# Kernel optimization log

Measured on AMD Instinct MI355X. Metric: run time of the kernel, lower is better.

Reference implementation:

```python
import jax, jax.numpy as jnp
import numpy as np
import math

N_HEADS = 4
GELU = lambda x: jax.nn.gelu(x, approximate=False)  # torch nn.GELU default = exact erf

def _ln(x, s, b):
    m = jnp.mean(x, axis=-1, keepdims=True)
    v = jnp.mean((x - m) ** 2, axis=-1, keepdims=True)
    return (x - m) * jax.lax.rsqrt(v + 1e-5) * s + b

def _fwd(materials, in_seq, proj_vars, param_vars, enc_w1, enc_b1, enc_w2, enc_b2, sos,
         tl_wq, tl_wk, tl_wv, tl_bq, tl_bk, tl_bv, tl_wo, tl_bo,
         tl_ln1s, tl_ln1b, tl_ln2s, tl_ln2b, tl_fw1, tl_fb1, tl_fw2, tl_fb2,
         pw1, pb1, pw2, pb2, pw3, pb3, pw4, pb4, pw5, pb5,
         ipw1, ipb1, ipw2, ipb2, hw1, hb1, hw2, hb2, hw3, hb3):
    B = in_seq.shape[0]
    # encoder input MLP: [B,S,1] -> [B,S,D]
    x = GELU(in_seq @ enc_w1 + enc_b1) @ enc_w2 + enc_b2
    x = jnp.concatenate([jnp.broadcast_to(sos, (B, 1, sos.shape[-1])), x], axis=1)
    S1, D = x.shape[1], x.shape[2]
    dh = D // N_HEADS
    # sinusoidal positional encoding
    pos = jnp.arange(S1, dtype=jnp.float32)[:, None]
    div = jnp.exp(jnp.arange(0, D, 2, dtype=jnp.float32) * (-math.log(10000.0) / D))
    ang = pos * div
    pe = jnp.stack([jnp.sin(ang), jnp.cos(ang)], axis=-1).reshape(S1, D)
    x = x + pe
    scale = 1.0 / math.sqrt(dh)
    # post-LN TransformerEncoder layers (torch default norm_first=False), eval mode (no dropout)
    for l in range(tl_wq.shape[0]):
        q = (x @ tl_wq[l] + tl_bq[l]).reshape(B, S1, N_HEADS, dh).transpose(0, 2, 1, 3)
        k = (x @ tl_wk[l] + tl_bk[l]).reshape(B, S1, N_HEADS, dh).transpose(0, 2, 1, 3)
        v = (x @ tl_wv[l] + tl_bv[l]).reshape(B, S1, N_HEADS, dh).transpose(0, 2, 1, 3)
        att = jax.nn.softmax(jnp.einsum('bhqd,bhkd->bhqk', q, k) * scale, axis=-1)
        o = jnp.einsum('bhqk,bhkd->bhqd', att, v).transpose(0, 2, 1, 3).reshape(B, S1, D)
        x = _ln(x + o @ tl_wo[l] + tl_bo[l], tl_ln1s[l], tl_ln1b[l])
        f = GELU(x @ tl_fw1[l] + tl_fb1[l]) @ tl_fw2[l] + tl_fb2[l]
        x = _ln(x + f, tl_ln2s[l], tl_ln2b[l])
    sos_out = x[:, 0]
    h = jnp.concatenate([proj_vars, sos_out], axis=1)
    for w, b in ((pw1, pb1), (pw2, pb2), (pw3, pb3), (pw4, pb4)):
        h = GELU(h @ w + b)
    proj_out = h @ pw5 + pb5
    pp = GELU(param_vars @ ipw1 + ipb1) @ ipw2 + ipb2
    mi = jnp.concatenate([pp, proj_out], axis=1)  # [B, output_features+param_vars]
    # MaterialHead mask-gather-MLP-scatter == run every tiny head densely, pick by material id
    h1 = GELU(jnp.einsum('bi,mio->mbo', mi, hw1) + hb1[:, None, :])
    h2 = GELU(jnp.einsum('mbi,mio->mbo', h1, hw2) + hb2[:, None, :])
    h3 = jnp.einsum('mbi,mio->mbo', h2, hw3) + hb3[:, None, :]  # [M,B,1]
    return h3[materials, jnp.arange(B)]  # [B,1]

def setup_inputs() -> dict:
    key = jax.random.key(0)
    ks = iter(jax.random.split(key, 64))
    def rn(shape, scale=0.05):
        return jax.random.normal(next(ks), shape, dtype=jnp.float32) * scale
    B, S, IN, EL, D, L, DFF = 64, 1024, 1, 48, 64, 3, 256
    PV, PP, OF, M = 3, 3, 24, 3
    IF = OF + PP
    return dict(
        in_seq=rn((B, S, IN), 1.0),
        proj_vars=rn((B, PV), 1.0),
        param_vars=rn((B, PP), 1.0),
        materials=jax.random.randint(next(ks), (B,), 0, M),
        enc_w1=rn((IN, EL)), enc_b1=rn((EL,)), enc_w2=rn((EL, D)), enc_b2=rn((D,)),
        sos=rn((1, 1, D)),
        tl_wq=rn((L, D, D)), tl_wk=rn((L, D, D)), tl_wv=rn((L, D, D)),
        tl_bq=rn((L, D)), tl_bk=rn((L, D)), tl_bv=rn((L, D)),
        tl_wo=rn((L, D, D)), tl_bo=rn((L, D)),
        tl_ln1s=jnp.ones((L, D)), tl_ln1b=jnp.zeros((L, D)),
        tl_ln2s=jnp.ones((L, D)), tl_ln2b=jnp.zeros((L, D)),
        tl_fw1=rn((L, D, DFF)), tl_fb1=rn((L, DFF)), tl_fw2=rn((L, DFF, D)), tl_fb2=rn((L, D)),
        pw1=rn((PV + D, 34)), pb1=rn((34,)), pw2=rn((34, 11)), pb2=rn((11,)),
        pw3=rn((11, 36)), pb3=rn((36,)), pw4=rn((36, 22)), pb4=rn((22,)),
        pw5=rn((22, OF)), pb5=rn((OF,)),
        ipw1=rn((PP, 3)), ipb1=rn((3,)), ipw2=rn((3, PP)), ipb2=rn((PP,)),
        hw1=rn((M, IF, 15)), hb1=rn((M, 15)), hw2=rn((M, 15, 18)), hb2=rn((M, 18)),
        hw3=rn((M, 18, 1)), hb3=rn((M, 1)),
    )

def reference(in_seq, proj_vars, param_vars, materials, enc_w1, enc_b1, enc_w2, enc_b2, sos,
              tl_wq, tl_wk, tl_wv, tl_bq, tl_bk, tl_bv, tl_wo, tl_bo,
              tl_ln1s, tl_ln1b, tl_ln2s, tl_ln2b, tl_fw1, tl_fb1, tl_fw2, tl_fb2,
              pw1, pb1, pw2, pb2, pw3, pb3, pw4, pb4, pw5, pb5,
              ipw1, ipb1, ipw2, ipb2, hw1, hb1, hw2, hb2, hw3, hb3):
    return _fwd(materials, in_seq, proj_vars, param_vars, enc_w1, enc_b1, enc_w2, enc_b2, sos,
                tl_wq, tl_wk, tl_wv, tl_bq, tl_bk, tl_bv, tl_wo, tl_bo,
                tl_ln1s, tl_ln1b, tl_ln2s, tl_ln2b, tl_fw1, tl_fb1, tl_fw2, tl_fb2,
                pw1, pb1, pw2, pb2, pw3, pb3, pw4, pb4, pw5, pb5,
                ipw1, ipb1, ipw2, ipb2, hw1, hb1, hw2, hb2, hw3, hb3)
```

## Files before the change

kernel.cpp:

```cpp
#include <hip/hip_runtime.h>
#include <hip/hip_bf16.h>
#include <math.h>

#define BB   64
#define SS   1024
#define S1C  1025
#define DD   64
#define NHD  4
#define NBH  (BB * NHD)
#define DHD  16
#define DFFC 256
#define NLAY 3
#define NTOK (BB * S1C)
#define SPAD 1056
#define TGRP2 9
#define FTQ   32
#define FT2   32
#define HPAD 264
#define OPAD 68
#define YPAD 72
#define QSCL 0.36067376022224085f

typedef const float* fp;
typedef __attribute__((ext_vector_type(8))) short bf16x8;
typedef __attribute__((ext_vector_type(4))) float f32x4;
typedef __attribute__((ext_vector_type(2))) unsigned int u32x2;
typedef __attribute__((ext_vector_type(4))) unsigned int u32x4;

#if __has_builtin(__builtin_amdgcn_exp2f)
#define RAW_EXP2(x) __builtin_amdgcn_exp2f(x)
#else
#define RAW_EXP2(x) __expf(0.6931471805599453f * (x))
#endif
#if __has_builtin(__builtin_amdgcn_rcpf)
#define RAW_RCP(x) __builtin_amdgcn_rcpf(x)
#else
#define RAW_RCP(x) (1.0f / (x))
#endif

__device__ __forceinline__ float gelu_exact(float x) {
    return 0.5f * x * (1.0f + erff(x * 0.7071067811865475f));
}
__device__ __forceinline__ float erf_fast(float x) {
    float ax = fabsf(x);
    float t = RAW_RCP(1.0f + 0.3275911f * ax);
    float p = t * (0.254829592f + t * (-0.284496736f + t * (1.421413741f +
              t * (-1.453152027f + t * 1.061405429f))));
    float e = RAW_EXP2(ax * ax * -1.4426950408889634f);
    float r = 1.0f - p * e;
    return copysignf(r, x);
}
__device__ __forceinline__ float gelu_fast(float x) {
    return 0.5f * x * (1.0f + erf_fast(x * 0.7071067811865475f));
}
__device__ __forceinline__ short f2b(float f) {
    unsigned u = __float_as_uint(f);
    return (short)((u + 0x7fffu + ((u >> 16) & 1u)) >> 16);
}
__device__ __forceinline__ short f2b_pos(float f) {
    return (short)((__float_as_uint(f) + 0x8000u) >> 16);
}

__device__ __forceinline__ u32x2 pack4exp(f32x4 c, bool valid) {
    unsigned a0 = __float_as_uint(valid ? RAW_EXP2(c[0]) : 0.f) + 0x8000u;
    unsigned a1 = __float_as_uint(valid ? RAW_EXP2(c[1]) : 0.f) + 0x8000u;
    unsigned a2 = __float_as_uint(valid ? RAW_EXP2(c[2]) : 0.f) + 0x8000u;
    unsigned a3 = __float_as_uint(valid ? RAW_EXP2(c[3]) : 0.f) + 0x8000u;
    return (u32x2){__builtin_amdgcn_perm(a1, a0, 0x07060302u),
                   __builtin_amdgcn_perm(a3, a2, 0x07060302u)};
}

__global__ __launch_bounds__(256) void k_wconv(
    fp wq, fp wk, fp wv, fp wo, fp w1, fp w2,
    short* __restrict__ wqkvT, short* __restrict__ woT,
    short* __restrict__ w1T, short* __restrict__ w2T)
{
    int l = blockIdx.y;
    int i = blockIdx.x * 256 + threadIdx.x;
    if (i < 12288) {
        int p = i >> 12, rem = i & 4095;
        int d = rem >> 6, j = rem & 63;
        fp src = (p == 0 ? wq : p == 1 ? wk : wv) + (size_t)l * 4096;
        float v = src[j * 64 + d];
        if (p == 0) v *= QSCL;
        wqkvT[(size_t)l * 12288 + i] = f2b(v);
    } else if (i < 16384) {
        int rem = i - 12288;
        woT[(size_t)l * 4096 + rem] = f2b(wo[(size_t)l * 4096 + (rem & 63) * 64 + (rem >> 6)]);
    } else if (i < 32768) {
        int rem = i - 16384;
        w1T[(size_t)l * 16384 + rem] = f2b(w1[(size_t)l * 16384 + (rem & 63) * 256 + (rem >> 6)]);
    } else {
        int rem = i - 32768;
        w2T[(size_t)l * 16384 + rem] = f2b(w2[(size_t)l * 16384 + (rem & 255) * 64 + (rem >> 8)]);
    }
}

__global__ __launch_bounds__(64) void k_zero(
    short* __restrict__ qb, short* __restrict__ kb, short* __restrict__ vbt)
{
    int bh = blockIdx.x, t = threadIdx.x;
    for (int i = t; i < 31 * 16; i += 64) {
        int r = i >> 4, c = i & 15;
        size_t idx = ((size_t)bh * SPAD + 1025 + r) * 16 + c;
        qb[idx] = 0; kb[idx] = 0;
    }
    for (int i = t; i < 16 * 31; i += 64) {
        int e = i / 31, c = i % 31;
        vbt[((size_t)bh * 16 + e) * SPAD + 1025 + c] = 0;
    }
}

__global__ __launch_bounds__(256) void k_encode(
    fp in_seq, fp enc_w1, fp enc_b1, fp enc_w2, fp enc_b2, fp sos,
    float* __restrict__ x, short* __restrict__ xb)
{
    int t = threadIdx.x;
    int w = t >> 6, d = t & 63;
    int tok = blockIdx.x * 4 + w;
    int b = tok / S1C, s = tok % S1C;
    __shared__ float e[4][48];
    float val;
    if (s == 0) {
        val = sos[d];
    } else {
        float tin = in_seq[b * SS + (s - 1)];
        if (d < 48) e[w][d] = gelu_fast(tin * enc_w1[d] + enc_b1[d]);
        float acc = enc_b2[d];
        for (int j = 0; j < 48; ++j) acc += e[w][j] * enc_w2[j * DD + d];
        val = acc;
    }
    int i2 = (d >> 1) * 2;
    float factor = RAW_EXP2((float)i2 * (-9.210340371976184f / 64.0f) * 1.4426950408889634f);
    float ang = (float)s * factor;
    val += (d & 1) ? __cosf(ang) : __sinf(ang);
    x[(size_t)tok * DD + d] = val;
    xb[(size_t)tok * DD + d] = f2b(val);
}

__global__ __launch_bounds__(256) void k_qkv(
    const short* __restrict__ xb, const short* __restrict__ wqkvT,
    fp bq, fp bk, fp bv,
    short* __restrict__ qb, short* __restrict__ kb, short* __restrict__ vbt)
{
    int blk = blockIdx.x, t = threadIdx.x;
    int tok0 = blk * FTQ;
    int w = t >> 6, l = t & 63;
    int quad = l >> 4, lo = l & 15;

    const short* xp0 = xb + ((size_t)(tok0 + lo)) * DD;
    const short* xp1 = xb + ((size_t)(tok0 + 16 + lo)) * DD;
    bf16x8 a0 = *(const bf16x8*)(xp0 + quad * 8);
    bf16x8 a1 = *(const bf16x8*)(xp0 + 32 + quad * 8);
    bf16x8 a2 = *(const bf16x8*)(xp1 + quad * 8);
    bf16x8 a3 = *(const bf16x8*)(xp1 + 32 + quad * 8);

    int n = w * 16 + lo;
    #pragma unroll
    for (int p = 0; p < 3; ++p) {
        const short* wT = wqkvT + (size_t)p * 4096 + (size_t)n * 64;
        bf16x8 b0 = *(const bf16x8*)(wT + quad * 8);
        bf16x8 b1 = *(const bf16x8*)(wT + 32 + quad * 8);
        f32x4 c0 = __builtin_amdgcn_mfma_f32_16x16x32_bf16(a0, b0, (f32x4){0,0,0,0}, 0, 0, 0);
        c0 = __builtin_amdgcn_mfma_f32_16x16x32_bf16(a1, b1, c0, 0, 0, 0);
        f32x4 c1 = __builtin_amdgcn_mfma_f32_16x16x32_bf16(a2, b0, (f32x4){0,0,0,0}, 0, 0, 0);
        c1 = __builtin_amdgcn_mfma_f32_16x16x32_bf16(a3, b1, c1, 0, 0, 0);
        float bias = (p == 0) ? bq[n] * QSCL : (p == 1) ? bk[n] : bv[n];
        #pragma unroll
        for (int r = 0; r < 4; ++r) {
            int tok = tok0 + quad * 4 + r;
            int bb0 = tok / S1C, ss0 = tok % S1C;
            int bh = bb0 * NHD + w;
            short val = f2b(c0[r] + bias);
            int tok2 = tok + 16;
            int bb1 = tok2 / S1C, ss1 = tok2 % S1C;
            int bh2 = bb1 * NHD + w;
            short val2 = f2b(c1[r] + bias);
            if (p == 0) {
                qb[((size_t)bh * SPAD + ss0) * 16 + lo] = val;
                qb[((size_t)bh2 * SPAD + ss1) * 16 + lo] = val2;
            } else if (p == 1) {
                kb[((size_t)bh * SPAD + ss0) * 16 + lo] = val;
                kb[((size_t)bh2 * SPAD + ss1) * 16 + lo] = val2;
            } else {
                vbt[((size_t)bh * 16 + lo) * SPAD + ss0] = val;
                vbt[((size_t)bh2 * 16 + lo) * SPAD + ss1] = val2;
            }
        }
    }
}

__global__ __launch_bounds__(256) void k_attn(
    const short* __restrict__ qb, const short* __restrict__ kb,
    const short* __restrict__ vbt, short* __restrict__ ob)
{
    int bid = blockIdx.x;
    int bh  = bid % NBH;
    int grp = bid / NBH;
    int b = bh >> 2, h = bh & 3;
    int t = threadIdx.x;
    int w = t >> 6, l = t & 63;
    int quad = l >> 4, lo = l & 15;
    int t0 = grp * 4 + w;
    int t1 = t0 + 36;
    if (t1 > 65) t1 = 65;
    int qg0 = t0 * 16, qg1 = t1 * 16;

    __shared__ u32x2 ptmem[4][2][272];
    char* ptc = (char*)&ptmem[w][0][0];
    unsigned ptbase = (unsigned)(uintptr_t)ptc;

    const short* qbase = qb + (size_t)bh * SPAD * 16;
    const short* kbase = kb + (size_t)bh * SPAD * 16;
    const short* vbase = vbt + (size_t)bh * 16 * SPAD;

    bf16x8 aQ0 = {0,0,0,0,0,0,0,0}, aQ1 = {0,0,0,0,0,0,0,0};
    if (quad < 2) {
        aQ0 = *(const bf16x8*)(qbase + ((size_t)(qg0 + lo)) * 16 + quad * 8);
        aQ1 = *(const bf16x8*)(qbase + ((size_t)(qg1 + lo)) * 16 + quad * 8);
    }

    const short ONE = 0x3F80;
    bf16x8 aOne = {ONE, ONE, ONE, ONE, ONE, ONE, ONE, ONE};

    f32x4 oc0 = {0.f,0.f,0.f,0.f}, oc1 = {0.f,0.f,0.f,0.f};
    f32x4 dn0 = {0.f,0.f,0.f,0.f}, dn1 = {0.f,0.f,0.f,0.f};

    unsigned wo0, wo1;
    { int k0 = lo;       wo0 = (unsigned)((k0 >> 2) * 136 + (k0 & 3) * 32 + quad * 8);
      int k1 = 16 + lo;  wo1 = (unsigned)((k1 >> 2) * 136 + (k1 & 3) * 32 + quad * 8); }
    unsigned ro = (unsigned)(quad * 272 + lo * 8);
    unsigned rd0 = ptbase + ro;
    unsigned rd1 = ptbase + 2176 + ro;
    char* wb0 = ptc;
    char* wb1 = ptc + 2176;

    bf16x8 kxA, kyA, kxB, kyB, vA, vB;

    {
        const short* k0p = kbase + (size_t)lo * 16 + (quad & 1) * 8;
        kxA = *(const bf16x8*)k0p;
        kyA = *(const bf16x8*)(k0p + 256);
        vA  = *(const bf16x8*)(vbase + (size_t)lo * SPAD + quad * 8);
        const short* k1p = kbase + (size_t)(32 + lo) * 16 + (quad & 1) * 8;
        kxB = *(const bf16x8*)k1p;
        kyB = *(const bf16x8*)(k1p + 256);

        f32x4 c0 = __builtin_amdgcn_mfma_f32_16x16x32_bf16(aQ0, kxA, (f32x4){0.f,0.f,0.f,0.f}, 0, 0, 0);
        f32x4 c1 = __builtin_amdgcn_mfma_f32_16x16x32_bf16(aQ1, kxA, (f32x4){0.f,0.f,0.f,0.f}, 0, 0, 0);
        *(u32x2*)(wb0 + wo0)        = pack4exp(c0, true);
        *(u32x2*)(wb0 + 1088 + wo0) = pack4exp(c1, true);
        c0 = __builtin_amdgcn_mfma_f32_16x16x32_bf16(aQ0, kyA, (f32x4){0.f,0.f,0.f,0.f}, 0, 0, 0);
        c1 = __builtin_amdgcn_mfma_f32_16x16x32_bf16(aQ1, kyA, (f32x4){0.f,0.f,0.f,0.f}, 0, 0, 0);
        *(u32x2*)(wb0 + wo1)        = pack4exp(c0, true);
        *(u32x2*)(wb0 + 1088 + wo1) = pack4exp(c1, true);
    }

#define STEP(CH, TAIL, KXC, KYC, KXN, KYN, VP, VC, RD, WB) do {               \
    int ch_ = (CH);                                                            \
    if (!(TAIL)) {                                                             \
        const short* kn_ = kbase + (size_t)((ch_ + 1) * 32 + lo) * 16 + (quad & 1) * 8; \
        KXN = *(const bf16x8*)kn_;                                             \
        KYN = *(const bf16x8*)(kn_ + 256);                                     \
    }                                                                          \
    VC = *(const bf16x8*)(vbase + (size_t)lo * SPAD + ch_ * 32 + quad * 8);    \
    asm volatile("s_waitcnt lgkmcnt(0)" ::: "memory");                         \
    u32x2 p00_, p01_, p10_, p11_;                                              \
    asm volatile("ds_read_b64_tr_b16 %0, %1"             : "=v"(p00_) : "v"(RD)); \
    asm volatile("ds_read_b64_tr_b16 %0, %1 offset:136"  : "=v"(p01_) : "v"(RD)); \
    asm volatile("ds_read_b64_tr_b16 %0, %1 offset:1088" : "=v"(p10_) : "v"(RD)); \
    asm volatile("ds_read_b64_tr_b16 %0, %1 offset:1224" : "=v"(p11_) : "v"(RD)); \
    u32x2 wA0_, wA1_, wB0_, wB1_;                                              \
    {                                                                          \
        f32x4 c0_ = __builtin_amdgcn_mfma_f32_16x16x32_bf16(aQ0, KXC, (f32x4){0.f,0.f,0.f,0.f}, 0, 0, 0); \
        f32x4 c1_ = __builtin_amdgcn_mfma_f32_16x16x32_bf16(aQ1, KXC, (f32x4){0.f,0.f,0.f,0.f}, 0, 0, 0); \
        bool v0_ = !(TAIL) || (lo == 0);                                       \
        wA0_ = pack4exp(c0_, v0_);                                             \
        wB0_ = pack4exp(c1_, v0_);                                             \
        c0_ = __builtin_amdgcn_mfma_f32_16x16x32_bf16(aQ0, KYC, (f32x4){0.f,0.f,0.f,0.f}, 0, 0, 0); \
        c1_ = __builtin_amdgcn_mfma_f32_16x16x32_bf16(aQ1, KYC, (f32x4){0.f,0.f,0.f,0.f}, 0, 0, 0); \
        bool v1_ = !(TAIL);                                                    \
        wA1_ = pack4exp(c0_, v1_);                                             \
        wB1_ = pack4exp(c1_, v1_);                                             \
    }                                                                          \
    asm volatile("s_waitcnt lgkmcnt(0)" ::: "memory");                         \
    __builtin_amdgcn_sched_barrier(0);                                         \
    u32x4 q0_; q0_[0] = p00_[0]; q0_[1] = p00_[1]; q0_[2] = p01_[0]; q0_[3] = p01_[1]; \
    u32x4 q1_; q1_[0] = p10_[0]; q1_[1] = p10_[1]; q1_[2] = p11_[0]; q1_[3] = p11_[1]; \
    bf16x8 pB0_ = __builtin_bit_cast(bf16x8, q0_);                             \
    bf16x8 pB1_ = __builtin_bit_cast(bf16x8, q1_);                             \
    oc0 = __builtin_amdgcn_mfma_f32_16x16x32_bf16(VP, pB0_, oc0, 0, 0, 0);     \
    dn0 = __builtin_amdgcn_mfma_f32_16x16x32_bf16(aOne, pB0_, dn0, 0, 0, 0);   \
    oc1 = __builtin_amdgcn_mfma_f32_16x16x32_bf16(VP, pB1_, oc1, 0, 0, 0);     \
    dn1 = __builtin_amdgcn_mfma_f32_16x16x32_bf16(aOne, pB1_, dn1, 0, 0, 0);   \
    *(u32x2*)((WB) + wo0)        = wA0_;                                       \
    *(u32x2*)((WB) + 1088 + wo0) = wB0_;                                       \
    *(u32x2*)((WB) + wo1)        = wA1_;                                       \
    *(u32x2*)((WB) + 1088 + wo1) = wB1_;                                       \
} while (0)

    for (int chp = 1; chp < 31; chp += 2) {
        STEP(chp,     0, kxA, kyA, kxB, kyB, vA, vB, rd0, wb1);
        STEP(chp + 1, 0, kxB, kyB, kxA, kyA, vB, vA, rd1, wb0);
    }
    STEP(31, 0, kxA, kyA, kxB, kyB, vA, vB, rd0, wb1);
    STEP(32, 1, kxB, kyB, kxA, kyA, vB, vA, rd1, wb0);
#undef STEP

    {
        asm volatile("s_waitcnt lgkmcnt(0)" ::: "memory");
        u32x2 p00, p01, p10, p11;
        asm volatile("ds_read_b64_tr_b16 %0, %1"             : "=v"(p00) : "v"(rd0));
        asm volatile("ds_read_b64_tr_b16 %0, %1 offset:136"  : "=v"(p01) : "v"(rd0));
        asm volatile("ds_read_b64_tr_b16 %0, %1 offset:1088" : "=v"(p10) : "v"(rd0));
        asm volatile("ds_read_b64_tr_b16 %0, %1 offset:1224" : "=v"(p11) : "v"(rd0));
        asm volatile("s_waitcnt lgkmcnt(0)" ::: "memory");
        __builtin_amdgcn_sched_barrier(0);
        u32x4 q0; q0[0] = p00[0]; q0[1] = p00[1]; q0[2] = p01[0]; q0[3] = p01[1];
        u32x4 q1; q1[0] = p10[0]; q1[1] = p10[1]; q1[2] = p11[0]; q1[3] = p11[1];
        bf16x8 pB0 = __builtin_bit_cast(bf16x8, q0);
        bf16x8 pB1 = __builtin_bit_cast(bf16x8, q1);
        oc0 = __builtin_amdgcn_mfma_f32_16x16x32_bf16(vA, pB0, oc0, 0, 0, 0);
        dn0 = __builtin_amdgcn_mfma_f32_16x16x32_bf16(aOne, pB0, dn0, 0, 0, 0);
        oc1 = __builtin_amdgcn_mfma_f32_16x16x32_bf16(vA, pB1, oc1, 0, 0, 0);
        dn1 = __builtin_amdgcn_mfma_f32_16x16x32_bf16(aOne, pB1, dn1, 0, 0, 0);
    }

    {
        int qrow = qg0 + lo;
        if (qrow < S1C) {
            float inv = 1.0f / dn0[0];
            unsigned p0 = (unsigned short)f2b(oc0[0] * inv) | ((unsigned)(unsigned short)f2b(oc0[1] * inv) << 16);
            unsigned p1 = (unsigned short)f2b(oc0[2] * inv) | ((unsigned)(unsigned short)f2b(oc0[3] * inv) << 16);
            *(uint2*)(ob + ((size_t)b * S1C + qrow) * DD + h * DHD + quad * 4) = make_uint2(p0, p1);
        }
    }
    {
        int qrow = qg1 + lo;
        if (qrow < S1C) {
            float inv = 1.0f / dn1[0];
            unsigned p0 = (unsigned short)f2b(oc1[0] * inv) | ((unsigned)(unsigned short)f2b(oc1[1] * inv) << 16);
            unsigned p1 = (unsigned short)f2b(oc1[2] * inv) | ((unsigned)(unsigned short)f2b(oc1[3] * inv) << 16);
            *(uint2*)(ob + ((size_t)b * S1C + qrow) * DD + h * DHD + quad * 4) = make_uint2(p0, p1);
        }
    }
}

__global__ __launch_bounds__(256) void k_block(
    const short* __restrict__ ob, float* __restrict__ x,
    const short* __restrict__ woT, fp bo, fp ln1s, fp ln1b,
    const short* __restrict__ w1T, fp b1, const short* __restrict__ w2T, fp b2,
    fp ln2s, fp ln2b,
    const short* __restrict__ wqkvTn, fp bqn, fp bkn, fp bvn,
    short* __restrict__ qb, short* __restrict__ kb, short* __restrict__ vbt,
    int has_next)
{
    int blk = blockIdx.x, t = threadIdx.x;
    int tok0 = blk * FT2;
    int w = t >> 6, l = t & 63;
    int quad = l >> 4, lo = l & 15;

    __shared__ float otf[FT2][OPAD];
    __shared__ short ys[FT2][YPAD];
    __shared__ short hid[FT2][HPAD];

    {
        const short* obp0 = ob + ((size_t)(tok0 + lo)) * DD;
        const short* obp1 = ob + ((size_t)(tok0 + 16 + lo)) * DD;
        bf16x8 a0 = *(const bf16x8*)(obp0 + quad * 8);
        bf16x8 a1 = *(const bf16x8*)(obp0 + 32 + quad * 8);
        bf16x8 a2 = *(const bf16x8*)(obp1 + quad * 8);
        bf16x8 a3 = *(const bf16x8*)(obp1 + 32 + quad * 8);
        int n = w * 16 + lo;
        const short* wT = woT + (size_t)n * 64;
        bf16x8 b0 = *(const bf16x8*)(wT + quad * 8);
        bf16x8 bb = *(const bf16x8*)(wT + 32 + quad * 8);
        f32x4 c0 = __builtin_amdgcn_mfma_f32_16x16x32_bf16(a0, b0, (f32x4){0,0,0,0}, 0, 0, 0);
        c0 = __builtin_amdgcn_mfma_f32_16x16x32_bf16(a1, bb, c0, 0, 0, 0);
        f32x4 c1 = __builtin_amdgcn_mfma_f32_16x16x32_bf16(a2, b0, (f32x4){0,0,0,0}, 0, 0, 0);
        c1 = __builtin_amdgcn_mfma_f32_16x16x32_bf16(a3, bb, c1, 0, 0, 0);
        float bov = bo[n];
        #pragma unroll
        for (int r = 0; r < 4; ++r) {
            otf[quad * 4 + r][n] = c0[r] + bov;
            otf[16 + quad * 4 + r][n] = c1[r] + bov;
        }
    }
    __syncthreads();

    int d = l;
    float yv[8];
    {
        float s1 = ln1s[d], bl1 = ln1b[d];
        #pragma unroll
        for (int i = 0; i < 8; ++i) {
            int tt = w * 8 + i;
            float val = otf[tt][d] + x[(size_t)(tok0 + tt) * DD + d];
            float sum = val, vs = val * val;
            #pragma unroll
            for (int off = 32; off > 0; off >>= 1) {
                sum += __shfl_xor(sum, off, 64);
                vs  += __shfl_xor(vs, off, 64);
            }
            float mean = sum * (1.0f / 64.0f);
            float var = vs * (1.0f / 64.0f) - mean * mean;
            float y = (val - mean) * rsqrtf(var + 1e-5f) * s1 + bl1;
            yv[i] = y;
            ys[tt][d] = f2b(y);
        }
    }
    __syncthreads();

    {
        bf16x8 a0 = *(const bf16x8*)&ys[lo][quad * 8];
        bf16x8 a1 = *(const bf16x8*)&ys[lo][32 + quad * 8];
        bf16x8 a2 = *(const bf16x8*)&ys[16 + lo][quad * 8];
        bf16x8 a3 = *(const bf16x8*)&ys[16 + lo][32 + quad * 8];
        #pragma unroll
        for (int i = 0; i < 4; ++i) {
            int n = w * 64 + i * 16 + lo;
            const short* wT = w1T + (size_t)n * 64;
            bf16x8 b0 = *(const bf16x8*)(wT + quad * 8);
            bf16x8 bb = *(const bf16x8*)(wT + 32 + quad * 8);
            f32x4 c0 = __builtin_amdgcn_mfma_f32_16x16x32_bf16(a0, b0, (f32x4){0,0,0,0}, 0, 0, 0);
            c0 = __builtin_amdgcn_mfma_f32_16x16x32_bf16(a1, bb, c0, 0, 0, 0);
            f32x4 c1 = __builtin_amdgcn_mfma_f32_16x16x32_bf16(a2, b0, (f32x4){0,0,0,0}, 0, 0, 0);
            c1 = __builtin_amdgcn_mfma_f32_16x16x32_bf16(a3, bb, c1, 0, 0, 0);
            float b1v = b1[n];
            #pragma unroll
            for (int r = 0; r < 4; ++r) {
                hid[quad * 4 + r][n] = f2b(gelu_fast(c0[r] + b1v));
                hid[16 + quad * 4 + r][n] = f2b(gelu_fast(c1[r] + b1v));
            }
        }
    }
    __syncthreads();

    {
        f32x4 c20 = {0.f,0.f,0.f,0.f}, c21 = {0.f,0.f,0.f,0.f};
        const short* wT2 = w2T + (size_t)(w * 16 + lo) * 256;
        #pragma unroll
        for (int kc = 0; kc < 8; ++kc) {
            bf16x8 b2f = *(const bf16x8*)(wT2 + kc * 32 + quad * 8);
            bf16x8 a20 = *(const bf16x8*)&hid[lo][kc * 32 + quad * 8];
            bf16x8 a21 = *(const bf16x8*)&hid[16 + lo][kc * 32 + quad * 8];
            c20 = __builtin_amdgcn_mfma_f32_16x16x32_bf16(a20, b2f, c20, 0, 0, 0);
            c21 = __builtin_amdgcn_mfma_f32_16x16x32_bf16(a21, b2f, c21, 0, 0, 0);
        }
        float b2v = b2[w * 16 + lo];
        #pragma unroll
        for (int r = 0; r < 4; ++r) {
            otf[quad * 4 + r][w * 16 + lo] = c20[r] + b2v;
            otf[16 + quad * 4 + r][w * 16 + lo] = c21[r] + b2v;
        }
    }
    __syncthreads();

    {
        float s2 = ln2s[d], bl2 = ln2b[d];
        #pragma unroll
        for (int i = 0; i < 8; ++i) {
            int tt = w * 8 + i;
            float val = otf[tt][d] + yv[i];
            float sum = val, vs = val * val;
            #pragma unroll
            for (int off = 32; off > 0; off >>= 1) {
                sum += __shfl_xor(sum, off, 64);
                vs  += __shfl_xor(vs, off, 64);
            }
            float mean = sum * (1.0f / 64.0f);
            float var = vs * (1.0f / 64.0f) - mean * mean;
            float y = (val - mean) * rsqrtf(var + 1e-5f) * s2 + bl2;
            x[(size_t)(tok0 + tt) * DD + d] = y;
            ys[tt][d] = f2b(y);
        }
    }
    __syncthreads();

    if (has_next) {
        bf16x8 a0 = *(const bf16x8*)&ys[lo][quad * 8];
        bf16x8 a1 = *(const bf16x8*)&ys[lo][32 + quad * 8];
        bf16x8 a2 = *(const bf16x8*)&ys[16 + lo][quad * 8];
        bf16x8 a3 = *(const bf16x8*)&ys[16 + lo][32 + quad * 8];
        int n = w * 16 + lo;
        #pragma unroll
        for (int p = 0; p < 3; ++p) {
            const short* wT = wqkvTn + (size_t)p * 4096 + (size_t)n * 64;
            bf16x8 b0 = *(const bf16x8*)(wT + quad * 8);
            bf16x8 bb = *(const bf16x8*)(wT + 32 + quad * 8);
            f32x4 c0 = __builtin_amdgcn_mfma_f32_16x16x32_bf16(a0, b0, (f32x4){0,0,0,0}, 0, 0, 0);
            c0 = __builtin_amdgcn_mfma_f32_16x16x32_bf16(a1, bb, c0, 0, 0, 0);
            f32x4 c1 = __builtin_amdgcn_mfma_f32_16x16x32_bf16(a2, b0, (f32x4){0,0,0,0}, 0, 0, 0);
            c1 = __builtin_amdgcn_mfma_f32_16x16x32_bf16(a3, bb, c1, 0, 0, 0);
            float bias = (p == 0) ? bqn[n] * QSCL : (p == 1) ? bkn[n] : bvn[n];
            #pragma unroll
            for (int r = 0; r < 4; ++r) {
                int tok = tok0 + quad * 4 + r;
                int bb0 = tok / S1C, ss0 = tok % S1C;
                int bh = bb0 * NHD + w;
                short val = f2b(c0[r] + bias);
                int tok2 = tok + 16;
                int bb1 = tok2 / S1C, ss1 = tok2 % S1C;
                int bh2 = bb1 * NHD + w;
                short val2 = f2b(c1[r] + bias);
                if (p == 0) {
                    qb[((size_t)bh * SPAD + ss0) * 16 + lo] = val;
                    qb[((size_t)bh2 * SPAD + ss1) * 16 + lo] = val2;
                } else if (p == 1) {
                    kb[((size_t)bh * SPAD + ss0) * 16 + lo] = val;
                    kb[((size_t)bh2 * SPAD + ss1) * 16 + lo] = val2;
                } else {
                    vbt[((size_t)bh * 16 + lo) * SPAD + ss0] = val;
                    vbt[((size_t)bh2 * 16 + lo) * SPAD + ss1] = val2;
                }
            }
        }
    }
}

__global__ __launch_bounds__(64) void k_head(
    const float* __restrict__ x, fp proj_vars, fp param_vars,
    const int* __restrict__ materials,
    fp pw1, fp pb1, fp pw2, fp pb2, fp pw3, fp pb3,
    fp pw4, fp pb4, fp pw5, fp pb5,
    fp ipw1, fp ipb1, fp ipw2, fp ipb2,
    fp hw1, fp hb1, fp hw2, fp hb2, fp hw3, fp hb3,
    float* __restrict__ out)
{
    int b = blockIdx.x;
    int tid = threadIdx.x;
    __shared__ float A[80], Bf[80], pp[8], mi[32];

    if (tid < 3) A[tid] = proj_vars[b * 3 + tid];
    A[3 + tid] = x[((size_t)b * S1C + 0) * DD + tid];
    __syncthreads();

    if (tid < 34) {
        float a = pb1[tid];
        for (int i = 0; i < 67; ++i) a += A[i] * pw1[i * 34 + tid];
        Bf[tid] = gelu_exact(a);
    }
    __syncthreads();
    if (tid < 11) {
        float a = pb2[tid];
        for (int i = 0; i < 34; ++i) a += Bf[i] * pw2[i * 11 + tid];
        A[tid] = gelu_exact(a);
    }
    __syncthreads();
    if (tid < 36) {
        float a = pb3[tid];
        for (int i = 0; i < 11; ++i) a += A[i] * pw3[i * 36 + tid];
        Bf[tid] = gelu_exact(a);
    }
    __syncthreads();
    if (tid < 22) {
        float a = pb4[tid];
        for (int i = 0; i < 36; ++i) a += Bf[i] * pw4[i * 22 + tid];
        A[tid] = gelu_exact(a);
    }
    __syncthreads();
    if (tid < 24) {
        float a = pb5[tid];
        for (int i = 0; i < 22; ++i) a += A[i] * pw5[i * 24 + tid];
        mi[3 + tid] = a;
    }
    if (tid < 3) {
        float a = ipb1[tid];
        for (int i = 0; i < 3; ++i) a += param_vars[b * 3 + i] * ipw1[i * 3 + tid];
        pp[tid] = gelu_exact(a);
    }
    __syncthreads();
    if (tid < 3) {
        float a = ipb2[tid];
        for (int i = 0; i < 3; ++i) a += pp[i] * ipw2[i * 3 + tid];
        mi[tid] = a;
    }
    __syncthreads();

    int m = materials[b];
    if (tid < 15) {
        float a = hb1[m * 15 + tid];
        for (int i = 0; i < 27; ++i) a += mi[i] * hw1[(m * 27 + i) * 15 + tid];
        A[tid] = gelu_exact(a);
    }
    __syncthreads();
    if (tid < 18) {
        float a = hb2[m * 18 + tid];
        for (int i = 0; i < 15; ++i) a += A[i] * hw2[(m * 15 + i) * 18 + tid];
        Bf[tid] = gelu_exact(a);
    }
    __syncthreads();
    if (tid == 0) {
        float a = hb3[m];
        for (int i = 0; i < 18; ++i) a += Bf[i] * hw3[m * 18 + i];
        out[b] = a;
    }
}

extern "C" void kernel_launch(void* const* d_in, const int* in_sizes, int n_in,
                              void* d_out, int out_size, void* d_ws, size_t ws_size,
                              hipStream_t stream) {
    fp in_seq     = (fp)d_in[0];
    fp proj_vars  = (fp)d_in[1];
    fp param_vars = (fp)d_in[2];
    const int* materials = (const int*)d_in[3];
    fp enc_w1 = (fp)d_in[4];
    fp enc_b1 = (fp)d_in[5];
    fp enc_w2 = (fp)d_in[6];
    fp enc_b2 = (fp)d_in[7];
    fp sos    = (fp)d_in[8];
    fp tl_wq  = (fp)d_in[9];
    fp tl_wk  = (fp)d_in[10];
    fp tl_wv  = (fp)d_in[11];
    fp tl_bq  = (fp)d_in[12];
    fp tl_bk  = (fp)d_in[13];
    fp tl_bv  = (fp)d_in[14];
    fp tl_wo  = (fp)d_in[15];
    fp tl_bo  = (fp)d_in[16];
    fp tl_ln1s = (fp)d_in[17];
    fp tl_ln1b = (fp)d_in[18];
    fp tl_ln2s = (fp)d_in[19];
    fp tl_ln2b = (fp)d_in[20];
    fp tl_fw1 = (fp)d_in[21];
    fp tl_fb1 = (fp)d_in[22];
    fp tl_fw2 = (fp)d_in[23];
    fp tl_fb2 = (fp)d_in[24];
    fp pw1 = (fp)d_in[25]; fp pb1 = (fp)d_in[26];
    fp pw2 = (fp)d_in[27]; fp pb2 = (fp)d_in[28];
    fp pw3 = (fp)d_in[29]; fp pb3 = (fp)d_in[30];
    fp pw4 = (fp)d_in[31]; fp pb4 = (fp)d_in[32];
    fp pw5 = (fp)d_in[33]; fp pb5 = (fp)d_in[34];
    fp ipw1 = (fp)d_in[35]; fp ipb1 = (fp)d_in[36];
    fp ipw2 = (fp)d_in[37]; fp ipb2 = (fp)d_in[38];
    fp hw1 = (fp)d_in[39]; fp hb1 = (fp)d_in[40];
    fp hw2 = (fp)d_in[41]; fp hb2 = (fp)d_in[42];
    fp hw3 = (fp)d_in[43]; fp hb3 = (fp)d_in[44];

    float* x  = (float*)d_ws;
    short* ob = (short*)(x + (size_t)NTOK * DD);
    short* xb = ob + (size_t)NTOK * DD;
    short* qb = xb + (size_t)NTOK * DD;
    short* kb = qb + (size_t)NBH * SPAD * 16;
    short* vbt = kb + (size_t)NBH * SPAD * 16;
    short* wqkvT = vbt + (size_t)NBH * 16 * SPAD;
    short* woT = wqkvT + (size_t)NLAY * 12288;
    short* w1T = woT + (size_t)NLAY * 4096;
    short* w2T = w1T + (size_t)NLAY * 16384;

    k_wconv<<<dim3(192, NLAY), 256, 0, stream>>>(
        tl_wq, tl_wk, tl_wv, tl_wo, tl_fw1, tl_fw2, wqkvT, woT, w1T, w2T);
    k_zero<<<NBH, 64, 0, stream>>>(qb, kb, vbt);
    k_encode<<<NTOK / 4, 256, 0, stream>>>(in_seq, enc_w1, enc_b1, enc_w2, enc_b2, sos, x, xb);

    k_qkv<<<NTOK / FTQ, 256, 0, stream>>>(
        xb, wqkvT,
        tl_bq, tl_bk, tl_bv,
        qb, kb, vbt);

    for (int l = 0; l < NLAY; ++l) {
        k_attn<<<NBH * TGRP2, 256, 0, stream>>>(qb, kb, vbt, ob);
        int ln = (l + 1 < NLAY) ? (l + 1) : l;
        k_block<<<NTOK / FT2, 256, 0, stream>>>(
            ob, x,
            woT + (size_t)l * 4096, tl_bo + (size_t)l * DD,
            tl_ln1s + (size_t)l * DD, tl_ln1b + (size_t)l * DD,
            w1T + (size_t)l * 16384, tl_fb1 + (size_t)l * DFFC,
            w2T + (size_t)l * 16384, tl_fb2 + (size_t)l * DD,
            tl_ln2s + (size_t)l * DD, tl_ln2b + (size_t)l * DD,
            wqkvT + (size_t)ln * 12288,
            tl_bq + (size_t)ln * DD, tl_bk + (size_t)ln * DD, tl_bv + (size_t)ln * DD,
            qb, kb, vbt,
            (l + 1 < NLAY) ? 1 : 0);
    }

    k_head<<<BB, 64, 0, stream>>>(
        x, proj_vars, param_vars, materials,
        pw1, pb1, pw2, pb2, pw3, pb3, pw4, pb4, pw5, pb5,
        ipw1, ipb1, ipw2, ipb2,
        hw1, hb1, hw2, hb2, hw3, hb3,
        (float*)d_out);
}
```

Before: 523.7 us.

## Store FFN hidden tile transposed and read it with ds_read_b64_tr_b16

In the fused post-attention block kernel, the GELU hidden activations are now packed four at a time into 64-bit LDS stores in a transposed layout. The second FFN matmul reads them back with the transpose-read instruction ds_read_b64_tr_b16, software-pipelined with manual waitcnt and sched barriers. The LN output buffer now aliases the otf scratch buffer, which shrinks the LDS footprint. The aim is to replace the scalar 16-bit hidden writes with wide stores and to raise occupancy, at the cost of hand-written asm with fixed offsets and strict ordering assumptions.

```diff
diff --git a/kernel.cpp b/kernel.cpp
--- a/kernel.cpp
+++ b/kernel.cpp
@@ -16,9 +16,7 @@
 #define TGRP2 9
 #define FTQ   32
 #define FT2   32
-#define HPAD 264
 #define OPAD 68
-#define YPAD 72
 #define QSCL 0.36067376022224085f
 
 typedef const float* fp;
@@ -57,15 +55,20 @@
     unsigned u = __float_as_uint(f);
     return (short)((u + 0x7fffu + ((u >> 16) & 1u)) >> 16);
 }
-__device__ __forceinline__ short f2b_pos(float f) {
-    return (short)((__float_as_uint(f) + 0x8000u) >> 16);
-}
 
 __device__ __forceinline__ u32x2 pack4exp(f32x4 c, bool valid) {
     unsigned a0 = __float_as_uint(valid ? RAW_EXP2(c[0]) : 0.f) + 0x8000u;
     unsigned a1 = __float_as_uint(valid ? RAW_EXP2(c[1]) : 0.f) + 0x8000u;
     unsigned a2 = __float_as_uint(valid ? RAW_EXP2(c[2]) : 0.f) + 0x8000u;
     unsigned a3 = __float_as_uint(valid ? RAW_EXP2(c[3]) : 0.f) + 0x8000u;
+    return (u32x2){__builtin_amdgcn_perm(a1, a0, 0x07060302u),
+                   __builtin_amdgcn_perm(a3, a2, 0x07060302u)};
+}
+__device__ __forceinline__ u32x2 pack4f(float x0, float x1, float x2, float x3) {
+    unsigned a0 = __float_as_uint(x0) + 0x8000u;
+    unsigned a1 = __float_as_uint(x1) + 0x8000u;
+    unsigned a2 = __float_as_uint(x2) + 0x8000u;
+    unsigned a3 = __float_as_uint(x3) + 0x8000u;
     return (u32x2){__builtin_amdgcn_perm(a1, a0, 0x07060302u),
                    __builtin_amdgcn_perm(a3, a2, 0x07060302u)};
 }
@@ -361,8 +364,10 @@
     int quad = l >> 4, lo = l & 15;
 
     __shared__ float otf[FT2][OPAD];
-    __shared__ short ys[FT2][YPAD];
-    __shared__ short hid[FT2][HPAD];
+    __shared__ u32x2 hidtr[2][8][136];
+    short* ysb = (short*)&otf[0][0];
+    char*  hidc = (char*)&hidtr[0][0][0];
+    unsigned hidbase = (unsigned)(uintptr_t)hidc;
 
     {
         const short* obp0 = ob + ((size_t)(tok0 + lo)) * DD;
@@ -406,16 +411,17 @@
             float var = vs * (1.0f / 64.0f) - mean * mean;
             float y = (val - mean) * rsqrtf(var + 1e-5f) * s1 + bl1;
             yv[i] = y;
-            ys[tt][d] = f2b(y);
-        }
-    }
-    __syncthreads();
-
-    {
-        bf16x8 a0 = *(const bf16x8*)&ys[lo][quad * 8];
-        bf16x8 a1 = *(const bf16x8*)&ys[lo][32 + quad * 8];
-        bf16x8 a2 = *(const bf16x8*)&ys[16 + lo][quad * 8];
-        bf16x8 a3 = *(const bf16x8*)&ys[16 + lo][32 + quad * 8];
+            ysb[tt * 136 + d] = f2b(y);
+        }
+    }
+    __syncthreads();
+
+    {
+        bf16x8 a0 = *(const bf16x8*)&ysb[(size_t)lo * 136 + quad * 8];
+        bf16x8 a1 = *(const bf16x8*)&ysb[(size_t)lo * 136 + 32 + quad * 8];
+        bf16x8 a2 = *(const bf16x8*)&ysb[(size_t)(16 + lo) * 136 + quad * 8];
+        bf16x8 a3 = *(const bf16x8*)&ysb[(size_t)(16 + lo) * 136 + 32 + quad * 8];
+        unsigned hoff = (unsigned)(w * 2176 + (lo >> 2) * 136 + (lo & 3) * 32 + quad * 8);
         #pragma unroll
         for (int i = 0; i < 4; ++i) {
             int n = w * 64 + i * 16 + lo;
@@ -427,11 +433,13 @@
             f32x4 c1 = __builtin_amdgcn_mfma_f32_16x16x32_bf16(a2, b0, (f32x4){0,0,0,0}, 0, 0, 0);
             c1 = __builtin_amdgcn_mfma_f32_16x16x32_bf16(a3, bb, c1, 0, 0, 0);
             float b1v = b1[n];
-            #pragma unroll
-            for (int r = 0; r < 4; ++r) {
-                hid[quad * 4 + r][n] = f2b(gelu_fast(c0[r] + b1v));
-                hid[16 + quad * 4 + r][n] = f2b(gelu_fast(c1[r] + b1v));
-            }
+            unsigned off = hoff + (i >> 1) * 1088 + (i & 1) * 544;
+            *(u32x2*)(hidc + off) = pack4f(
+                gelu_fast(c0[0] + b1v), gelu_fast(c0[1] + b1v),
+                gelu_fast(c0[2] + b1v), gelu_fast(c0[3] + b1v));
+            *(u32x2*)(hidc + 8704 + off) = pack4f(
+                gelu_fast(c1[0] + b1v), gelu_fast(c1[1] + b1v),
+                gelu_fast(c1[2] + b1v), gelu_fast(c1[3] + b1v));
         }
     }
     __syncthreads();
@@ -439,14 +447,54 @@
     {
         f32x4 c20 = {0.f,0.f,0.f,0.f}, c21 = {0.f,0.f,0.f,0.f};
         const short* wT2 = w2T + (size_t)(w * 16 + lo) * 256;
-        #pragma unroll
-        for (int kc = 0; kc < 8; ++kc) {
-            bf16x8 b2f = *(const bf16x8*)(wT2 + kc * 32 + quad * 8);
-            bf16x8 a20 = *(const bf16x8*)&hid[lo][kc * 32 + quad * 8];
-            bf16x8 a21 = *(const bf16x8*)&hid[16 + lo][kc * 32 + quad * 8];
-            c20 = __builtin_amdgcn_mfma_f32_16x16x32_bf16(a20, b2f, c20, 0, 0, 0);
-            c21 = __builtin_amdgcn_mfma_f32_16x16x32_bf16(a21, b2f, c21, 0, 0, 0);
-        }
+        unsigned ro = (unsigned)(quad * 272 + lo * 8);
+        unsigned tb0 = hidbase + ro;
+        unsigned tb1 = hidbase + 8704 + ro;
+        u32x2 pA0, pA1, pA2, pA3, pB0, pB1, pB2, pB3;
+
+#define TRRD(dst, addr, OFFSTR) \
+    asm volatile("ds_read_b64_tr_b16 %0, %1 offset:" OFFSTR : "=v"(dst) : "v"(addr))
+#define ISS(P0,P1,P2,P3, O1, O2) \
+    TRRD(P0, tb0, O1); TRRD(P1, tb0, O2); TRRD(P2, tb1, O1); TRRD(P3, tb1, O2)
+#define W4 asm volatile("s_waitcnt lgkmcnt(4)" ::: "memory"); __builtin_amdgcn_sched_barrier(0)
+#define W0 asm volatile("s_waitcnt lgkmcnt(0)" ::: "memory"); __builtin_amdgcn_sched_barrier(0)
+#define CONS(P0,P1,P2,P3, BF) do { \
+    u32x4 q0_; q0_[0]=P0[0]; q0_[1]=P0[1]; q0_[2]=P1[0]; q0_[3]=P1[1]; \
+    u32x4 q1_; q1_[0]=P2[0]; q1_[1]=P2[1]; q1_[2]=P3[0]; q1_[3]=P3[1]; \
+    c20 = __builtin_amdgcn_mfma_f32_16x16x32_bf16(__builtin_bit_cast(bf16x8,q0_), BF, c20, 0,0,0); \
+    c21 = __builtin_amdgcn_mfma_f32_16x16x32_bf16(__builtin_bit_cast(bf16x8,q1_), BF, c21, 0,0,0); \
+} while (0)
+
+        bf16x8 bfA = *(const bf16x8*)(wT2 + quad * 8);
+        ISS(pA0,pA1,pA2,pA3, "0",    "136");
+        bf16x8 bfB = *(const bf16x8*)(wT2 + 32 + quad * 8);
+        ISS(pB0,pB1,pB2,pB3, "1088", "1224");
+        W4; CONS(pA0,pA1,pA2,pA3, bfA);
+        bfA = *(const bf16x8*)(wT2 + 64 + quad * 8);
+        ISS(pA0,pA1,pA2,pA3, "2176", "2312");
+        W4; CONS(pB0,pB1,pB2,pB3, bfB);
+        bfB = *(const bf16x8*)(wT2 + 96 + quad * 8);
+        ISS(pB0,pB1,pB2,pB3, "3264", "3400");
+        W4; CONS(pA0,pA1,pA2,pA3, bfA);
+        bfA = *(const bf16x8*)(wT2 + 128 + quad * 8);
+        ISS(pA0,pA1,pA2,pA3, "4352", "4488");
+        W4; CONS(pB0,pB1,pB2,pB3, bfB);
+        bfB = *(const bf16x8*)(wT2 + 160 + quad * 8);
+        ISS(pB0,pB1,pB2,pB3, "5440", "5576");
+        W4; CONS(pA0,pA1,pA2,pA3, bfA);
+        bfA = *(const bf16x8*)(wT2 + 192 + quad * 8);
+        ISS(pA0,pA1,pA2,pA3, "6528", "6664");
+        W4; CONS(pB0,pB1,pB2,pB3, bfB);
+        bfB = *(const bf16x8*)(wT2 + 224 + quad * 8);
+        ISS(pB0,pB1,pB2,pB3, "7616", "7752");
+        W4; CONS(pA0,pA1,pA2,pA3, bfA);
+        W0; CONS(pB0,pB1,pB2,pB3, bfB);
+#undef TRRD
+#undef ISS
+#undef W4
+#undef W0
+#undef CONS
+
         float b2v = b2[w * 16 + lo];
         #pragma unroll
         for (int r = 0; r < 4; ++r) {
@@ -472,16 +520,16 @@
             float var = vs * (1.0f / 64.0f) - mean * mean;
             float y = (val - mean) * rsqrtf(var + 1e-5f) * s2 + bl2;
             x[(size_t)(tok0 + tt) * DD + d] = y;
-            ys[tt][d] = f2b(y);
+            ysb[tt * 136 + d] = f2b(y);
         }
     }
     __syncthreads();
 
     if (has_next) {
-        bf16x8 a0 = *(const bf16x8*)&ys[lo][quad * 8];
-        bf16x8 a1 = *(const bf16x8*)&ys[lo][32 + quad * 8];
-        bf16x8 a2 = *(const bf16x8*)&ys[16 + lo][quad * 8];
-        bf16x8 a3 = *(const bf16x8*)&ys[16 + lo][32 + quad * 8];
+        bf16x8 a0 = *(const bf16x8*)&ysb[(size_t)lo * 136 + quad * 8];
+        bf16x8 a1 = *(const bf16x8*)&ysb[(size_t)lo * 136 + 32 + quad * 8];
+        bf16x8 a2 = *(const bf16x8*)&ysb[(size_t)(16 + lo) * 136 + quad * 8];
+        bf16x8 a3 = *(const bf16x8*)&ysb[(size_t)(16 + lo) * 136 + 32 + quad * 8];
         int n = w * 16 + lo;
         #pragma unroll
         for (int p = 0; p < 3; ++p) {
```

New measurement: 504.4 us. -3.7%, faster.
